# Performance work log

Measured on AMD Instinct MI355X. Metric: run time of the kernel, lower is better.

Reference implementation:

```python
import jax, jax.numpy as jnp
import numpy as np

N_NODES = 65536
N_EDGES = 1048576
DIM = 64
N_GRAPHS = 16


def setup_inputs() -> dict:
    key = jax.random.key(0)
    ks = jax.random.split(key, 8)
    node_feats = jax.random.normal(ks[0], (N_NODES, DIM), dtype=jnp.float32)
    edge_index = jax.random.randint(ks[1], (2, N_EDGES), 0, N_NODES, dtype=jnp.int32)
    batch_num_nodes = jnp.full((N_GRAPHS,), N_NODES // N_GRAPHS, dtype=jnp.int32)
    s = 1.0 / np.sqrt(DIM)
    W1 = jax.random.normal(ks[2], (DIM, DIM), dtype=jnp.float32) * s
    W2 = jax.random.normal(ks[3], (DIM, DIM), dtype=jnp.float32) * s
    W3 = jax.random.normal(ks[4], (DIM, DIM), dtype=jnp.float32) * s
    b1 = jnp.zeros((DIM,), jnp.float32)
    b2 = jnp.zeros((DIM,), jnp.float32)
    b3 = jnp.zeros((DIM,), jnp.float32)
    return {"node_feats": node_feats, "edge_index": edge_index,
            "batch_num_nodes": batch_num_nodes,
            "W1": W1, "b1": b1, "W2": W2, "b2": b2, "W3": W3, "b3": b3}


def _graph_conv(x, src, dst, W, b, n_nodes):
    # DGL GraphConv with norm='both': D_out^{-1/2} A^T D_in^{-1/2} style sym norm
    ones = jnp.ones((src.shape[0],), x.dtype)
    deg_out = jnp.clip(jax.ops.segment_sum(ones, src, num_segments=n_nodes), 1.0)
    deg_in = jnp.clip(jax.ops.segment_sum(ones, dst, num_segments=n_nodes), 1.0)
    h = x * jax.lax.rsqrt(deg_out)[:, None]          # [N, d] scale by src out-deg
    agg = jax.ops.segment_sum(h[src], dst, num_segments=n_nodes)  # gather+scatter
    agg = agg * jax.lax.rsqrt(deg_in)[:, None]
    return agg @ W + b


def _unbatch(h, batch_num_nodes):
    # pad each graph's node block to max_num_node -> [B, max_n, d]
    bnn = np.asarray(batch_num_nodes)
    B = bnn.shape[0]
    max_n = int(bnn.max())
    offsets = np.concatenate([[0], np.cumsum(bnn)])
    graph_id = np.repeat(np.arange(B), bnn)                 # [N_total]
    pos = np.arange(int(offsets[-1])) - offsets[graph_id]   # position within graph
    out = jnp.zeros((B, max_n, h.shape[1]), h.dtype)
    return out.at[jnp.asarray(graph_id), jnp.asarray(pos)].set(h)


def reference(node_feats, edge_index, batch_num_nodes, W1, b1, W2, b2, W3, b3):
    src, dst = edge_index[0], edge_index[1]
    n = node_feats.shape[0]
    h = jax.nn.relu(_graph_conv(node_feats, src, dst, W1, b1, n))
    h = jax.nn.relu(_graph_conv(h, src, dst, W2, b2, n))
    h = _graph_conv(h, src, dst, W3, b3, n)
    return _unbatch(h, batch_num_nodes)
```

## Files before the change

### kernel.cpp

```cpp
#include <hip/hip_runtime.h>
#include <hip/hip_fp16.h>


#define N_NODES 65536
#define N_EDGES 1048576
#define DIM 64

#define CHUNKS 256
#define EPC (N_EDGES / CHUNKS)
#define HB 128
#define OH_WORDS 16384

struct alignas(8) h4 { __half2 a, b; };

__global__ void edge_hist(const int* __restrict__ src, const int* __restrict__ dst,
                          int* __restrict__ block_hist, unsigned* __restrict__ partial,
                          uint2* __restrict__ zeroA, uint2* __restrict__ zeroB) {
    __shared__ unsigned h[OH_WORDS];
    __shared__ int bh[2][256];
    int t = threadIdx.x;
    int j = blockIdx.x;
    for (int i = t; i < OH_WORDS; i += 256) h[i] = 0;
    bh[0][t] = 0; bh[1][t] = 0;
    __syncthreads();
    if (j == 0) {
        if (t < 16) zeroA[t] = make_uint2(0u, 0u);
        else if (t < 32) zeroB[t - 16] = make_uint2(0u, 0u);
    }
    int base = j * (2 * EPC);
    for (int i = t; i < 2 * EPC; i += 256) {
        int s = src[base + i];
        int d = dst[base + i];
        atomicAdd(&h[s >> 2], 1u << ((s & 3) * 8));
        atomicAdd(&bh[i >> 12][d >> 8], 1);
    }
    __syncthreads();
    unsigned* dp = partial + (size_t)j * OH_WORDS;
    for (int i = t; i < OH_WORDS; i += 256) dp[i] = h[i];
    block_hist[t * CHUNKS + 2 * j]     = bh[0][t];
    block_hist[t * CHUNKS + 2 * j + 1] = bh[1][t];
}

__global__ void part_scan(const int* __restrict__ bh, int* __restrict__ so) {
    __shared__ int s[1024];
    int t = threadIdx.x;
    const int4* b4 = (const int4*)(bh + t * 64);
    int4 v[16];
    int sum = 0;
    #pragma unroll
    for (int i = 0; i < 16; i++) {
        v[i] = b4[i];
        sum += v[i].x + v[i].y + v[i].z + v[i].w;
    }
    s[t] = sum;
    __syncthreads();
    for (int off = 1; off < 1024; off <<= 1) {
        int u = (t >= off) ? s[t - off] : 0;
        __syncthreads();
        s[t] += u;
        __syncthreads();
    }
    int run = s[t] - sum;
    int* o = so + t * 64;
    #pragma unroll
    for (int i = 0; i < 16; i++) {
        o[4 * i + 0] = run; run += v[i].x;
        o[4 * i + 1] = run; run += v[i].y;
        o[4 * i + 2] = run; run += v[i].z;
        o[4 * i + 3] = run; run += v[i].w;
    }
}

__global__ void part_scatter(const int* __restrict__ src, const int* __restrict__ dst,
                             const int* __restrict__ so, int* __restrict__ bpack) {
    __shared__ int cur[256];
    cur[threadIdx.x] = so[threadIdx.x * CHUNKS + blockIdx.x];
    __syncthreads();
    int base = blockIdx.x * EPC;
    for (int i = threadIdx.x; i < EPC; i += 256) {
        int s = src[base + i];
        int d = dst[base + i];
        int pos = atomicAdd(&cur[d >> 8], 1);
        bpack[pos] = s | ((d & 255) << 16);
    }
}

__global__ void bucket_fused(const int* __restrict__ bpack, const int* __restrict__ so,
                             int* __restrict__ row_start, float* __restrict__ rs_in,
                             unsigned short* __restrict__ csr_src) {
    __shared__ int stage[8192];
    __shared__ int h[256], sc[256], cur[256];
    int b = blockIdx.x;
    int t = threadIdx.x;
    int beg = so[b * CHUNKS];
    int end = (b == 255) ? N_EDGES : so[(b + 1) * CHUNKS];
    int n = end - beg;
    h[t] = 0;
    __syncthreads();
    for (int i = t; i < n; i += 256) {
        int p = bpack[beg + i];
        if (i < 8192) stage[i] = p;
        atomicAdd(&h[(p >> 16) & 255], 1);
    }
    __syncthreads();
    int d = h[t];
    sc[t] = d;
    __syncthreads();
    for (int off = 1; off < 256; off <<= 1) {
        int v = (t >= off) ? sc[t - off] : 0;
        __syncthreads();
        sc[t] += v;
        __syncthreads();
    }
    int rsv = beg + sc[t] - d;
    int node = b * 256 + t;
    row_start[node] = rsv;
    rs_in[node] = rsqrtf(d < 1 ? 1.0f : (float)d);
    if (node == N_NODES - 1) row_start[N_NODES] = N_EDGES;
    cur[t] = rsv;
    __syncthreads();
    for (int i = t; i < n; i += 256) {
        int p = (i < 8192) ? stage[i] : bpack[beg + i];
        int pos = atomicAdd(&cur[(p >> 16) & 255], 1);
        csr_src[pos] = (unsigned short)(p & 0xFFFF);
    }
}

__global__ void oh2p_prescale(const unsigned* __restrict__ partial,
                              float* __restrict__ rs_out,
                              const float4* __restrict__ x4, h4* __restrict__ xs) {
    __shared__ float rsl[256];
    int b = blockIdx.x;
    int t = threadIdx.x;
    if (t < 64) {
        int w = b * 64 + t;
        int c0 = 0, c1 = 0, c2 = 0, c3 = 0;
        for (int c = 0; c < HB; c++) {
            unsigned v = partial[(size_t)c * OH_WORDS + w];
            c0 += (int)(v & 255u);
            c1 += (int)((v >> 8) & 255u);
            c2 += (int)((v >> 16) & 255u);
            c3 += (int)(v >> 24);
        }
        float4 r = make_float4(rsqrtf(c0 < 1 ? 1.0f : (float)c0),
                               rsqrtf(c1 < 1 ? 1.0f : (float)c1),
                               rsqrtf(c2 < 1 ? 1.0f : (float)c2),
                               rsqrtf(c3 < 1 ? 1.0f : (float)c3));
        ((float4*)rs_out)[w] = r;
        rsl[t * 4 + 0] = r.x; rsl[t * 4 + 1] = r.y;
        rsl[t * 4 + 2] = r.z; rsl[t * 4 + 3] = r.w;
    }
    __syncthreads();
    int rowbase = b * 4096;
    for (int i = t; i < 4096; i += 256) {
        float r = rsl[i >> 4];
        float4 v = x4[rowbase + i];
        h4 o;
        o.a = __float22half2_rn(make_float2(v.x * r, v.y * r));
        o.b = __float22half2_rn(make_float2(v.z * r, v.w * r));
        xs[rowbase + i] = o;
    }
}

template<bool SCALE_OUT>
__global__ void fused_layer(const uint4* __restrict__ xs16, const int* __restrict__ row_start,
                            const unsigned short* __restrict__ csr,
                            const float* __restrict__ rs_out, const float* __restrict__ rs_in,
                            const float* __restrict__ W, const float* __restrict__ b,
                            void* __restrict__ outp) {
    __shared__ float4 Ws4[DIM * 16];
    __shared__ float4 bs4[16];
    {
        const float4* Wg = (const float4*)W;
        for (int i = threadIdx.x; i < DIM * 16; i += blockDim.x) Ws4[i] = Wg[i];
        if (threadIdx.x < 16) bs4[threadIdx.x] = ((const float4*)b)[threadIdx.x];
    }
    __syncthreads();

    int wave_id = threadIdx.x >> 6;
    int lane = threadIdx.x & 63;
    int g = lane >> 3;
    int l = lane & 7;
    int node = blockIdx.x * 32 + wave_id * 8 + g;

    int beg = row_start[node];
    int end = row_start[node + 1];

    float a0 = 0.f, a1 = 0.f, a2 = 0.f, a3 = 0.f,
          a4 = 0.f, a5 = 0.f, a6 = 0.f, a7 = 0.f;
    for (int k = beg; k < end; k += 8) {
        int s[8];
        #pragma unroll
        for (int j = 0; j < 8; j++) {
            int kk = k + j;
            int idx = csr[kk];
            s[j] = (kk < end) ? idx : N_NODES;
        }
        uint4 v[8];
        #pragma unroll
        for (int j = 0; j < 8; j++) v[j] = xs16[s[j] * 8 + l];
        #pragma unroll
        for (int j = 0; j < 8; j++) {
            float2 f0 = __half22float2(*(const __half2*)&v[j].x);
            float2 f1 = __half22float2(*(const __half2*)&v[j].y);
            float2 f2 = __half22float2(*(const __half2*)&v[j].z);
            float2 f3 = __half22float2(*(const __half2*)&v[j].w);
            a0 += f0.x; a1 += f0.y; a2 += f1.x; a3 += f1.y;
            a4 += f2.x; a5 += f2.y; a6 += f3.x; a7 += f3.y;
        }
    }
    float ri = rs_in[node];
    a0 *= ri; a1 *= ri; a2 *= ri; a3 *= ri;
    a4 *= ri; a5 *= ri; a6 *= ri; a7 *= ri;

    float4 o0 = bs4[2 * l];
    float4 o1 = bs4[2 * l + 1];
    int gbase = g << 3;
    #pragma unroll
    for (int m = 0; m < 8; m++) {
        float q0 = __shfl(a0, gbase + m, 64);
        float q1 = __shfl(a1, gbase + m, 64);
        float q2 = __shfl(a2, gbase + m, 64);
        float q3 = __shfl(a3, gbase + m, 64);
        float q4 = __shfl(a4, gbase + m, 64);
        float q5 = __shfl(a5, gbase + m, 64);
        float q6 = __shfl(a6, gbase + m, 64);
        float q7 = __shfl(a7, gbase + m, 64);
        int rb = (8 * m) * 16 + 2 * l;
        float4 w;
        w = Ws4[rb];            o0.x += q0*w.x; o0.y += q0*w.y; o0.z += q0*w.z; o0.w += q0*w.w;
        w = Ws4[rb + 1];        o1.x += q0*w.x; o1.y += q0*w.y; o1.z += q0*w.z; o1.w += q0*w.w;
        w = Ws4[rb + 16];       o0.x += q1*w.x; o0.y += q1*w.y; o0.z += q1*w.z; o0.w += q1*w.w;
        w = Ws4[rb + 17];       o1.x += q1*w.x; o1.y += q1*w.y; o1.z += q1*w.z; o1.w += q1*w.w;
        w = Ws4[rb + 32];       o0.x += q2*w.x; o0.y += q2*w.y; o0.z += q2*w.z; o0.w += q2*w.w;
        w = Ws4[rb + 33];       o1.x += q2*w.x; o1.y += q2*w.y; o1.z += q2*w.z; o1.w += q2*w.w;
        w = Ws4[rb + 48];       o0.x += q3*w.x; o0.y += q3*w.y; o0.z += q3*w.z; o0.w += q3*w.w;
        w = Ws4[rb + 49];       o1.x += q3*w.x; o1.y += q3*w.y; o1.z += q3*w.z; o1.w += q3*w.w;
        w = Ws4[rb + 64];       o0.x += q4*w.x; o0.y += q4*w.y; o0.z += q4*w.z; o0.w += q4*w.w;
        w = Ws4[rb + 65];       o1.x += q4*w.x; o1.y += q4*w.y; o1.z += q4*w.z; o1.w += q4*w.w;
        w = Ws4[rb + 80];       o0.x += q5*w.x; o0.y += q5*w.y; o0.z += q5*w.z; o0.w += q5*w.w;
        w = Ws4[rb + 81];       o1.x += q5*w.x; o1.y += q5*w.y; o1.z += q5*w.z; o1.w += q5*w.w;
        w = Ws4[rb + 96];       o0.x += q6*w.x; o0.y += q6*w.y; o0.z += q6*w.z; o0.w += q6*w.w;
        w = Ws4[rb + 97];       o1.x += q6*w.x; o1.y += q6*w.y; o1.z += q6*w.z; o1.w += q6*w.w;
        w = Ws4[rb + 112];      o0.x += q7*w.x; o0.y += q7*w.y; o0.z += q7*w.z; o0.w += q7*w.w;
        w = Ws4[rb + 113];      o1.x += q7*w.x; o1.y += q7*w.y; o1.z += q7*w.z; o1.w += q7*w.w;
    }
    if (SCALE_OUT) {
        float ro = rs_out[node];
        o0.x = (o0.x < 0.f ? 0.f : o0.x) * ro;
        o0.y = (o0.y < 0.f ? 0.f : o0.y) * ro;
        o0.z = (o0.z < 0.f ? 0.f : o0.z) * ro;
        o0.w = (o0.w < 0.f ? 0.f : o0.w) * ro;
        o1.x = (o1.x < 0.f ? 0.f : o1.x) * ro;
        o1.y = (o1.y < 0.f ? 0.f : o1.y) * ro;
        o1.z = (o1.z < 0.f ? 0.f : o1.z) * ro;
        o1.w = (o1.w < 0.f ? 0.f : o1.w) * ro;
        uint4 ho;
        *(__half2*)&ho.x = __float22half2_rn(make_float2(o0.x, o0.y));
        *(__half2*)&ho.y = __float22half2_rn(make_float2(o0.z, o0.w));
        *(__half2*)&ho.z = __float22half2_rn(make_float2(o1.x, o1.y));
        *(__half2*)&ho.w = __float22half2_rn(make_float2(o1.z, o1.w));
        ((uint4*)outp)[node * 8 + l] = ho;
    } else {
        float4* o4 = (float4*)outp;
        o4[node * 16 + 2 * l]     = o0;
        o4[node * 16 + 2 * l + 1] = o1;
    }
}

extern "C" void kernel_launch(void* const* d_in, const int* in_sizes, int n_in,
                              void* d_out, int out_size, void* d_ws, size_t ws_size,
                              hipStream_t stream) {
    const float* x   = (const float*)d_in[0];
    const int*   ei  = (const int*)d_in[1];
    const int*   src = ei;
    const int*   dst = ei + N_EDGES;
    const float* W1 = (const float*)d_in[3];
    const float* b1 = (const float*)d_in[4];
    const float* W2 = (const float*)d_in[5];
    const float* b2 = (const float*)d_in[6];
    const float* W3 = (const float*)d_in[7];
    const float* b3 = (const float*)d_in[8];
    float* out = (float*)d_out;

    char* ws = (char*)d_ws;
    float* rs        = (float*)ws;
    float* rs_out    = rs;
    float* rs_in     = rs + N_NODES;
    int*   row_start = (int*)(rs + 2 * N_NODES);
    int*   block_h   = row_start + (N_NODES + 256);
    int*   so        = block_h + 256 * CHUNKS;
    unsigned short* csr_src = (unsigned short*)(so + 256 * CHUNKS);
    h4*    bufA      = (h4*)(csr_src + N_EDGES + 16);
    h4*    bufB      = bufA + (size_t)(N_NODES + 1) * 16;
    unsigned* partial = (unsigned*)(bufB + (size_t)(N_NODES + 1) * 16);
    int*   bpack     = (int*)bufB;
    uint2* zeroA     = (uint2*)(bufA + (size_t)N_NODES * 16);
    uint2* zeroB     = (uint2*)(bufB + (size_t)N_NODES * 16);

    const int fb = N_NODES / 32;

    edge_hist    <<<HB, 256, 0, stream>>>(src, dst, block_h, partial, zeroA, zeroB);
    part_scan    <<<1, 1024, 0, stream>>>(block_h, so);
    part_scatter <<<CHUNKS, 256, 0, stream>>>(src, dst, so, bpack);
    bucket_fused <<<256, 256, 0, stream>>>(bpack, so, row_start, rs_in, csr_src);
    oh2p_prescale<<<256, 256, 0, stream>>>(partial, rs_out, (const float4*)x, bufA);

    fused_layer<true ><<<fb, 256, 0, stream>>>((const uint4*)bufA, row_start, csr_src, rs_out, rs_in, W1, b1, (void*)bufB);
    fused_layer<true ><<<fb, 256, 0, stream>>>((const uint4*)bufB, row_start, csr_src, rs_out, rs_in, W2, b2, (void*)bufA);
    fused_layer<false><<<fb, 256, 0, stream>>>((const uint4*)bufA, row_start, csr_src, rs_out, rs_in, W3, b3, (void*)out);
}
```

Before: 248.5 us.

## Merge partition scan into prescale kernel and double edge_hist block count

Runs edge_hist with 256 blocks, each covering one chunk, instead of 128 blocks covering two chunks each, so more CUs take part in the histogram pass. The single-block partition scan is folded into block 0 of the out-degree reduction and prescale kernel, which removes one launch. The prescale work now moves before part_scatter, and bpack is moved into the partial buffer region so bufB is not overwritten. In exchange, the out-degree reduction reads twice as many partial histograms, and block 0 of the merged kernel carries the serial scan with a large per-thread register array.

Measured after the change: 264.1 us. 1.06x slower.

```diff
diff --git a/kernel.cpp b/kernel.cpp
--- a/kernel.cpp
+++ b/kernel.cpp
@@ -8,7 +8,6 @@
 
 #define CHUNKS 256
 #define EPC (N_EDGES / CHUNKS)
-#define HB 128
 #define OH_WORDS 16384
 
 struct alignas(8) h4 { __half2 a, b; };
@@ -17,57 +16,94 @@
                           int* __restrict__ block_hist, unsigned* __restrict__ partial,
                           uint2* __restrict__ zeroA, uint2* __restrict__ zeroB) {
     __shared__ unsigned h[OH_WORDS];
-    __shared__ int bh[2][256];
+    __shared__ int bh[256];
     int t = threadIdx.x;
     int j = blockIdx.x;
     for (int i = t; i < OH_WORDS; i += 256) h[i] = 0;
-    bh[0][t] = 0; bh[1][t] = 0;
+    bh[t] = 0;
     __syncthreads();
     if (j == 0) {
         if (t < 16) zeroA[t] = make_uint2(0u, 0u);
         else if (t < 32) zeroB[t - 16] = make_uint2(0u, 0u);
     }
-    int base = j * (2 * EPC);
-    for (int i = t; i < 2 * EPC; i += 256) {
+    int base = j * EPC;
+    for (int i = t; i < EPC; i += 256) {
         int s = src[base + i];
         int d = dst[base + i];
         atomicAdd(&h[s >> 2], 1u << ((s & 3) * 8));
-        atomicAdd(&bh[i >> 12][d >> 8], 1);
+        atomicAdd(&bh[d >> 8], 1);
     }
     __syncthreads();
     unsigned* dp = partial + (size_t)j * OH_WORDS;
     for (int i = t; i < OH_WORDS; i += 256) dp[i] = h[i];
-    block_hist[t * CHUNKS + 2 * j]     = bh[0][t];
-    block_hist[t * CHUNKS + 2 * j + 1] = bh[1][t];
-}
-
-__global__ void part_scan(const int* __restrict__ bh, int* __restrict__ so) {
-    __shared__ int s[1024];
+    block_hist[t * CHUNKS + j] = bh[t];
+}
+
+__global__ void prescale_scan(const int* __restrict__ bhist, int* __restrict__ so,
+                              const unsigned* __restrict__ partial,
+                              float* __restrict__ rs_out,
+                              const float4* __restrict__ x4, h4* __restrict__ xs) {
+    __shared__ float rsl[256];
+    __shared__ int sscan[256];
+    int b = blockIdx.x;
     int t = threadIdx.x;
-    const int4* b4 = (const int4*)(bh + t * 64);
-    int4 v[16];
-    int sum = 0;
-    #pragma unroll
-    for (int i = 0; i < 16; i++) {
-        v[i] = b4[i];
-        sum += v[i].x + v[i].y + v[i].z + v[i].w;
-    }
-    s[t] = sum;
-    __syncthreads();
-    for (int off = 1; off < 1024; off <<= 1) {
-        int u = (t >= off) ? s[t - off] : 0;
+
+    if (b == 0) {
+        const int4* b4 = (const int4*)(bhist + t * CHUNKS);
+        int4 v[64];
+        int sum = 0;
+        #pragma unroll 8
+        for (int i = 0; i < 64; i++) {
+            v[i] = b4[i];
+            sum += v[i].x + v[i].y + v[i].z + v[i].w;
+        }
+        sscan[t] = sum;
         __syncthreads();
-        s[t] += u;
+        for (int off = 1; off < 256; off <<= 1) {
+            int u2 = (t >= off) ? sscan[t - off] : 0;
+            __syncthreads();
+            sscan[t] += u2;
+            __syncthreads();
+        }
+        int run = sscan[t] - sum;
+        int* o = so + t * CHUNKS;
+        #pragma unroll 8
+        for (int i = 0; i < 64; i++) {
+            o[4 * i + 0] = run; run += v[i].x;
+            o[4 * i + 1] = run; run += v[i].y;
+            o[4 * i + 2] = run; run += v[i].z;
+            o[4 * i + 3] = run; run += v[i].w;
+        }
         __syncthreads();
     }
-    int run = s[t] - sum;
-    int* o = so + t * 64;
-    #pragma unroll
-    for (int i = 0; i < 16; i++) {
-        o[4 * i + 0] = run; run += v[i].x;
-        o[4 * i + 1] = run; run += v[i].y;
-        o[4 * i + 2] = run; run += v[i].z;
-        o[4 * i + 3] = run; run += v[i].w;
+
+    if (t < 64) {
+        int w = b * 64 + t;
+        int c0 = 0, c1 = 0, c2 = 0, c3 = 0;
+        for (int c = 0; c < CHUNKS; c++) {
+            unsigned v = partial[(size_t)c * OH_WORDS + w];
+            c0 += (int)(v & 255u);
+            c1 += (int)((v >> 8) & 255u);
+            c2 += (int)((v >> 16) & 255u);
+            c3 += (int)(v >> 24);
+        }
+        float4 r = make_float4(rsqrtf(c0 < 1 ? 1.0f : (float)c0),
+                               rsqrtf(c1 < 1 ? 1.0f : (float)c1),
+                               rsqrtf(c2 < 1 ? 1.0f : (float)c2),
+                               rsqrtf(c3 < 1 ? 1.0f : (float)c3));
+        ((float4*)rs_out)[w] = r;
+        rsl[t * 4 + 0] = r.x; rsl[t * 4 + 1] = r.y;
+        rsl[t * 4 + 2] = r.z; rsl[t * 4 + 3] = r.w;
+    }
+    __syncthreads();
+    int rowbase = b * 4096;
+    for (int i = t; i < 4096; i += 256) {
+        float r = rsl[i >> 4];
+        float4 v = x4[rowbase + i];
+        h4 o;
+        o.a = __float22half2_rn(make_float2(v.x * r, v.y * r));
+        o.b = __float22half2_rn(make_float2(v.z * r, v.w * r));
+        xs[rowbase + i] = o;
     }
 }
 
@@ -123,42 +159,6 @@
         int p = (i < 8192) ? stage[i] : bpack[beg + i];
         int pos = atomicAdd(&cur[(p >> 16) & 255], 1);
         csr_src[pos] = (unsigned short)(p & 0xFFFF);
-    }
-}
-
-__global__ void oh2p_prescale(const unsigned* __restrict__ partial,
-                              float* __restrict__ rs_out,
-                              const float4* __restrict__ x4, h4* __restrict__ xs) {
-    __shared__ float rsl[256];
-    int b = blockIdx.x;
-    int t = threadIdx.x;
-    if (t < 64) {
-        int w = b * 64 + t;
-        int c0 = 0, c1 = 0, c2 = 0, c3 = 0;
-        for (int c = 0; c < HB; c++) {
-            unsigned v = partial[(size_t)c * OH_WORDS + w];
-            c0 += (int)(v & 255u);
-            c1 += (int)((v >> 8) & 255u);
-            c2 += (int)((v >> 16) & 255u);
-            c3 += (int)(v >> 24);
-        }
-        float4 r = make_float4(rsqrtf(c0 < 1 ? 1.0f : (float)c0),
-                               rsqrtf(c1 < 1 ? 1.0f : (float)c1),
-                               rsqrtf(c2 < 1 ? 1.0f : (float)c2),
-                               rsqrtf(c3 < 1 ? 1.0f : (float)c3));
-        ((float4*)rs_out)[w] = r;
-        rsl[t * 4 + 0] = r.x; rsl[t * 4 + 1] = r.y;
-        rsl[t * 4 + 2] = r.z; rsl[t * 4 + 3] = r.w;
-    }
-    __syncthreads();
-    int rowbase = b * 4096;
-    for (int i = t; i < 4096; i += 256) {
-        float r = rsl[i >> 4];
-        float4 v = x4[rowbase + i];
-        h4 o;
-        o.a = __float22half2_rn(make_float2(v.x * r, v.y * r));
-        o.b = __float22half2_rn(make_float2(v.z * r, v.w * r));
-        xs[rowbase + i] = o;
     }
 }
 
@@ -294,17 +294,17 @@
     h4*    bufA      = (h4*)(csr_src + N_EDGES + 16);
     h4*    bufB      = bufA + (size_t)(N_NODES + 1) * 16;
     unsigned* partial = (unsigned*)(bufB + (size_t)(N_NODES + 1) * 16);
-    int*   bpack     = (int*)bufB;
+    int*   bpack     = (int*)partial;
     uint2* zeroA     = (uint2*)(bufA + (size_t)N_NODES * 16);
     uint2* zeroB     = (uint2*)(bufB + (size_t)N_NODES * 16);
 
     const int fb = N_NODES / 32;
 
-    edge_hist    <<<HB, 256, 0, stream>>>(src, dst, block_h, partial, zeroA, zeroB);
-    part_scan    <<<1, 1024, 0, stream>>>(block_h, so);
+    edge_hist    <<<CHUNKS, 256, 0, stream>>>(src, dst, block_h, partial, zeroA, zeroB);
+    prescale_scan<<<CHUNKS, 256, 0, stream>>>(block_h, so, partial, rs_out,
+                                              (const float4*)x, bufA);
     part_scatter <<<CHUNKS, 256, 0, stream>>>(src, dst, so, bpack);
-    bucket_fused <<<256, 256, 0, stream>>>(bpack, so, row_start, rs_in, csr_src);
-    oh2p_prescale<<<256, 256, 0, stream>>>(partial, rs_out, (const float4*)x, bufA);
+    bucket_fused <<<CHUNKS, 256, 0, stream>>>(bpack, so, row_start, rs_in, csr_src);
 
     fused_layer<true ><<<fb, 256, 0, stream>>>((const uint4*)bufA, row_start, csr_src, rs_out, rs_in, W1, b1, (void*)bufB);
     fused_layer<true ><<<fb, 256, 0, stream>>>((const uint4*)bufB, row_start, csr_src, rs_out, rs_in, W2, b2, (void*)bufA);
```
